# Performance work log

Measured on AMD Instinct MI355X. Metric: run time of the kernel, lower is better.

The kernel has to match this reference:

```python
import jax, jax.numpy as jnp
import numpy as np

B, M, N, C = 8, 4096, 4096, 3


def setup_inputs() -> dict:
    key = jax.random.key(0)
    k1, k2 = jax.random.split(key)
    set1 = jax.random.normal(k1, (B, M, C), dtype=jnp.float32)
    set2 = jax.random.normal(k2, (B, N, C), dtype=jnp.float32)
    return {"set1": set1, "set2": set2}


def _pairwise_dist(set1, set2):
    # ||a - b|| computed via expansion to avoid a (B,M,N,C) broadcast tensor.
    sq1 = jnp.sum(set1 * set1, axis=-1)  # (B, M)
    sq2 = jnp.sum(set2 * set2, axis=-1)  # (B, N)
    inner = jnp.einsum("bmc,bnc->bmn", set1, set2)  # (B, M, N)
    d2 = sq1[:, :, None] + sq2[:, None, :] - 2.0 * inner
    return jnp.sqrt(jnp.maximum(d2, 0.0))  # (B, M, N)


def reference(set1, set2):
    # Average (Chamfer-style) Hausdorff: mean of directed nearest-neighbor
    # distances in both directions, summed.  Output shape (B,).
    d = _pairwise_dist(set1, set2)                # (B, M, N)
    term_1 = jnp.mean(jnp.min(d, axis=2), axis=1)  # set1 -> set2
    term_2 = jnp.mean(jnp.min(d, axis=1), axis=1)  # set2 -> set1
    res = term_1 + term_2
    if res.shape[0] == 1:
        res = jnp.squeeze(res, axis=0)
    return res
```

## Files before the change

kernel.cpp:

```cpp
#include <hip/hip_runtime.h>
#include <hip/hip_bf16.h>
#include <math.h>

constexpr int NB   = 8;
constexpr int NPTS = 4096;
constexpr int NSEG = 4;
constexpr int NN   = NPTS / NSEG;

typedef __attribute__((ext_vector_type(8)))  short  short8;
typedef __attribute__((ext_vector_type(16))) float  f32x16;

__device__ inline unsigned short f2bf(float v) {
    __hip_bfloat16 t = __float2bfloat16(v);
    return *reinterpret_cast<unsigned short*>(&t);
}
__device__ inline float bf2f(unsigned short u) {
    __hip_bfloat16 t = *reinterpret_cast<__hip_bfloat16*>(&u);
    return __bfloat162float(t);
}

__global__ __launch_bounds__(256, 4) void mfma_min_kernel(
    const float* __restrict__ s1, const float* __restrict__ s2,
    float* __restrict__ pmin)
{
    __shared__ short8 blds[2048];

    int bid  = blockIdx.x;
    int nseg = bid & 3;
    int qb   = (bid >> 2) & 15;
    int g    = bid >> 6;
    int b    = g & 7, dir = g >> 3;

    const float* Q    = dir ? s2 : s1;
    const float* Tset = dir ? s1 : s2;

    int tid = threadIdx.x;
    int wid = tid >> 6, l = tid & 63;
    int c = l & 31, h = l >> 5;

    const float* tsrc = Tset + ((size_t)b * NPTS + (size_t)nseg * NN) * 3;
    #pragma unroll
    for (int k = 0; k < 4; ++k) {
        int p = k * 256 + tid;
        float x = tsrc[p*3+0], y = tsrc[p*3+1], z = tsrc[p*3+2];
        float sq = fmaf(z, z, fmaf(y, y, x * x));
        float tx = -2.0f*x, ty = -2.0f*y, tz = -2.0f*z;
        unsigned short thx = f2bf(tx), thy = f2bf(ty), thz = f2bf(tz);
        unsigned short tlx = f2bf(tx - bf2f(thx));
        unsigned short tly = f2bf(ty - bf2f(thy));
        unsigned short tlz = f2bf(tz - bf2f(thz));
        unsigned short sqh = f2bf(sq);
        unsigned short sql = f2bf(sq - bf2f(sqh));
        short8 tLo = {(short)thx,(short)thy,(short)thz,(short)thx,(short)thy,(short)thz,(short)sqh,(short)sql};
        short8 tHi = {(short)tlx,(short)tly,(short)tlz,0,0,0,0,0};
        int slot = (p >> 5) * 64 + (p & 31);
        blds[slot]      = tLo;
        blds[slot + 32] = tHi;
    }

    short8 qfr[2]; float qx[2], qy[2], qz[2];
    #pragma unroll
    for (int f = 0; f < 2; ++f) {
        int qidx = qb * 256 + wid * 64 + f * 32 + c;
        const float* qp = Q + ((size_t)b * NPTS + qidx) * 3;
        float x = qp[0], y = qp[1], z = qp[2];
        qx[f] = x; qy[f] = y; qz[f] = z;
        unsigned short ahx = f2bf(x), ahy = f2bf(y), ahz = f2bf(z);
        if (h == 0) {
            unsigned short alx = f2bf(x - bf2f(ahx));
            unsigned short aly = f2bf(y - bf2f(ahy));
            unsigned short alz = f2bf(z - bf2f(ahz));
            unsigned short one = 0x3F80;
            qfr[f] = short8{(short)ahx,(short)ahy,(short)ahz,
                            (short)alx,(short)aly,(short)alz,(short)one,(short)one};
        } else {
            qfr[f] = short8{(short)ahx,(short)ahy,(short)ahz,0,0,0,0,0};
        }
    }
    __syncthreads();

    f32x16 zero, acc0, acc1;
    #pragma unroll
    for (int r = 0; r < 16; ++r) { zero[r] = 0.0f; acc0[r] = 3.4e38f; acc1[r] = 3.4e38f; }

    for (int i = 0; i < 16; ++i) {
        short8 t0 = blds[(2*i  ) * 64 + l];
        short8 t1 = blds[(2*i+1) * 64 + l];
        {
            f32x16 d0 = __builtin_amdgcn_mfma_f32_32x32x16_bf16(t0, qfr[0], zero, 0, 0, 0);
            f32x16 d1 = __builtin_amdgcn_mfma_f32_32x32x16_bf16(t1, qfr[0], zero, 0, 0, 0);
            #pragma unroll
            for (int r = 0; r < 16; ++r)
                acc0[r] = fminf(fminf(acc0[r], d0[r]), d1[r]);
        }
        {
            f32x16 d0 = __builtin_amdgcn_mfma_f32_32x32x16_bf16(t0, qfr[1], zero, 0, 0, 0);
            f32x16 d1 = __builtin_amdgcn_mfma_f32_32x32x16_bf16(t1, qfr[1], zero, 0, 0, 0);
            #pragma unroll
            for (int r = 0; r < 16; ++r)
                acc1[r] = fminf(fminf(acc1[r], d0[r]), d1[r]);
        }
    }

    float* pg = pmin + ((size_t)g * NSEG + nseg) * NPTS;
    #pragma unroll
    for (int f = 0; f < 2; ++f) {
        f32x16& a = f ? acc1 : acc0;
        float v = a[0];
        #pragma unroll
        for (int r = 1; r < 16; ++r) v = fminf(v, a[r]);
        v = fminf(v, __shfl_xor(v, 32, 64));
        if (h == 0) {
            float sa = fmaf(qz[f], qz[f], fmaf(qy[f], qy[f], qx[f] * qx[f]));
            pg[qb * 256 + wid * 64 + f * 32 + c] = sa + v;
        }
    }
}

__global__ __launch_bounds__(1024) void reduce_kernel(
    const float* __restrict__ pmin, float* __restrict__ out)
{
    int b = blockIdx.x;
    int t = threadIdx.x;

    float sum = 0.0f;
    #pragma unroll
    for (int dir = 0; dir < 2; ++dir) {
        const float4* pg = reinterpret_cast<const float4*>(
            pmin + (size_t)(dir * NB + b) * NSEG * NPTS) + t;
        float4 m = pg[0];
        #pragma unroll
        for (int s = 1; s < NSEG; ++s) {
            float4 v = pg[(size_t)s * 1024];
            m.x = fminf(m.x, v.x); m.y = fminf(m.y, v.y);
            m.z = fminf(m.z, v.z); m.w = fminf(m.w, v.w);
        }
        sum += sqrtf(fmaxf(m.x, 0.0f)) + sqrtf(fmaxf(m.y, 0.0f))
             + sqrtf(fmaxf(m.z, 0.0f)) + sqrtf(fmaxf(m.w, 0.0f));
    }

    for (int off = 32; off > 0; off >>= 1)
        sum += __shfl_down(sum, off, 64);

    __shared__ float red[16];
    if ((t & 63) == 0) red[t >> 6] = sum;
    __syncthreads();
    if (t == 0) {
        float tt = 0.0f;
        #pragma unroll
        for (int w = 0; w < 16; ++w) tt += red[w];
        out[b] = tt * (1.0f / (float)NPTS);
    }
}

extern "C" void kernel_launch(void* const* d_in, const int* in_sizes, int n_in,
                              void* d_out, int out_size, void* d_ws, size_t ws_size,
                              hipStream_t stream) {
    const float* set1 = (const float*)d_in[0];
    const float* set2 = (const float*)d_in[1];
    float* out  = (float*)d_out;
    float* pmin = (float*)d_ws;

    mfma_min_kernel<<<16 * 16 * NSEG, 256, 0, stream>>>(set1, set2, pmin);
    reduce_kernel<<<NB, 1024, 0, stream>>>(pmin, out);
}
```

Before: 17.69 us.

## Fuse min-reduction and mean into main kernel using atomics and last-block counters

The separate reduce kernel is replaced by a single fused kernel. Per-query partial minima are merged with atomicMin on order-preserving integer keys. Counters pick the last segment block for each query tile, which takes square roots and writes a tile sum, and the last tile block of all, which writes the final per-batch outputs. A hipMemsetAsync initialises the workspace each call, so there is still an extra stream operation, and correctness relies on atomic visibility without explicit fences.

```diff
diff --git a/kernel.cpp b/kernel.cpp
--- a/kernel.cpp
+++ b/kernel.cpp
@@ -19,11 +19,25 @@
     return __bfloat162float(t);
 }
 
-__global__ __launch_bounds__(256, 4) void mfma_min_kernel(
+__device__ inline unsigned fkey(float f) {
+    unsigned b = __float_as_uint(f);
+    return ((int)b < 0) ? ~b : (b | 0x80000000u);
+}
+__device__ inline float unfkey(unsigned k) {
+    unsigned b = (k & 0x80000000u) ? (k & 0x7FFFFFFFu) : ~k;
+    return __uint_as_float(b);
+}
+
+__global__ __launch_bounds__(256, 4) void hausdorff_kernel(
     const float* __restrict__ s1, const float* __restrict__ s2,
-    float* __restrict__ pmin)
+    unsigned* __restrict__ pmin, unsigned* __restrict__ ctr1,
+    unsigned* __restrict__ ctr2, float* __restrict__ ssum,
+    float* __restrict__ out)
 {
     __shared__ short8 blds[2048];
+    __shared__ float red[4];
+    __shared__ float gsum[16];
+    __shared__ unsigned flag;
 
     int bid  = blockIdx.x;
     int nseg = bid & 3;
@@ -102,7 +116,6 @@
         }
     }
 
-    float* pg = pmin + ((size_t)g * NSEG + nseg) * NPTS;
     #pragma unroll
     for (int f = 0; f < 2; ++f) {
         f32x16& a = f ? acc1 : acc0;
@@ -112,44 +125,52 @@
         v = fminf(v, __shfl_xor(v, 32, 64));
         if (h == 0) {
             float sa = fmaf(qz[f], qz[f], fmaf(qy[f], qy[f], qx[f] * qx[f]));
-            pg[qb * 256 + wid * 64 + f * 32 + c] = sa + v;
+            int q = qb * 256 + wid * 64 + f * 32 + c;
+            atomicMin(&pmin[(unsigned)g * NPTS + q], fkey(sa + v));
         }
     }
-}
 
-__global__ __launch_bounds__(1024) void reduce_kernel(
-    const float* __restrict__ pmin, float* __restrict__ out)
-{
-    int b = blockIdx.x;
-    int t = threadIdx.x;
+    __syncthreads();
+    if (tid == 0) {
+        unsigned old = atomicAdd(&ctr1[g * 16 + qb], 1u);
+        flag = (old == 2u) ? 1u : 0u;
+    }
+    __syncthreads();
+    if (!flag) return;
 
-    float sum = 0.0f;
-    #pragma unroll
-    for (int dir = 0; dir < 2; ++dir) {
-        const float4* pg = reinterpret_cast<const float4*>(
-            pmin + (size_t)(dir * NB + b) * NSEG * NPTS) + t;
-        float4 m = pg[0];
-        #pragma unroll
-        for (int s = 1; s < NSEG; ++s) {
-            float4 v = pg[(size_t)s * 1024];
-            m.x = fminf(m.x, v.x); m.y = fminf(m.y, v.y);
-            m.z = fminf(m.z, v.z); m.w = fminf(m.w, v.w);
+    {
+        int q = qb * 256 + tid;
+        unsigned key = atomicMin(&pmin[(unsigned)g * NPTS + q], 0xFFFFFFFFu);
+        float d2 = unfkey(key);
+        float s = sqrtf(fmaxf(d2, 0.0f));
+        for (int off = 32; off > 0; off >>= 1)
+            s += __shfl_down(s, off, 64);
+        if (l == 0) red[wid] = s;
+        __syncthreads();
+        if (tid == 0) {
+            float tot = red[0] + red[1] + red[2] + red[3];
+            atomicExch(&ssum[g * 16 + qb], tot);
         }
-        sum += sqrtf(fmaxf(m.x, 0.0f)) + sqrtf(fmaxf(m.y, 0.0f))
-             + sqrtf(fmaxf(m.z, 0.0f)) + sqrtf(fmaxf(m.w, 0.0f));
+        __syncthreads();
+        if (tid == 0) {
+            unsigned old2 = atomicAdd(ctr2, 1u);
+            flag = (old2 == 254u) ? 1u : 0u;
+        }
+        __syncthreads();
+        if (!flag) return;
     }
 
-    for (int off = 32; off > 0; off >>= 1)
-        sum += __shfl_down(sum, off, 64);
-
-    __shared__ float red[16];
-    if ((t & 63) == 0) red[t >> 6] = sum;
-    __syncthreads();
-    if (t == 0) {
-        float tt = 0.0f;
-        #pragma unroll
-        for (int w = 0; w < 16; ++w) tt += red[w];
-        out[b] = tt * (1.0f / (float)NPTS);
+    {
+        unsigned kb = atomicOr(reinterpret_cast<unsigned*>(&ssum[tid]), 0u);
+        float val = __uint_as_float(kb);
+        val += __shfl_xor(val, 1, 64);
+        val += __shfl_xor(val, 2, 64);
+        val += __shfl_xor(val, 4, 64);
+        val += __shfl_xor(val, 8, 64);
+        if ((tid & 15) == 0) gsum[tid >> 4] = val;
+        __syncthreads();
+        if (tid < NB)
+            out[tid] = (gsum[tid] + gsum[tid + 8]) * (1.0f / (float)NPTS);
     }
 }
 
@@ -158,9 +179,16 @@
                               hipStream_t stream) {
     const float* set1 = (const float*)d_in[0];
     const float* set2 = (const float*)d_in[1];
-    float* out  = (float*)d_out;
-    float* pmin = (float*)d_ws;
+    float* out = (float*)d_out;
 
-    mfma_min_kernel<<<16 * 16 * NSEG, 256, 0, stream>>>(set1, set2, pmin);
-    reduce_kernel<<<NB, 1024, 0, stream>>>(pmin, out);
+    unsigned char* ws = (unsigned char*)d_ws;
+    unsigned* ctr1 = (unsigned*)ws;
+    unsigned* ctr2 = (unsigned*)(ws + 1024);
+    float*    ssum = (float*)(ws + 1088);
+    unsigned* pmin = (unsigned*)(ws + 4096);
+
+    hipMemsetAsync(ws, 0xFF, 4096 + (size_t)2 * NB * NPTS * 4, stream);
+
+    hausdorff_kernel<<<16 * 16 * NSEG, 256, 0, stream>>>(
+        set1, set2, pmin, ctr1, ctr2, ssum, out);
 }
```

New measurement: 22.00 us. 1.24x slower.
